# Performance work log

Hardware: AMD Instinct MI355X
Metric: run time of the kernel (lower is better)

The kernel has to match this reference:

```python
import jax, jax.numpy as jnp
import numpy as np
import math

# Instant-NGP hash grid config (matches init_kwargs)
L = 16            # num_levels
F = 2             # feature_dim
T = 524288        # table_size (2**19) per level
N_MIN = 16
N_MAX = 2048
N_PTS = 524288    # number of query points

# spatial-hash primes from Instant-NGP / tiny-cuda-nn
PRIMES = jnp.array([1, 2654435761, 805459861], dtype=jnp.uint32)


def setup_inputs() -> dict:
    key = jax.random.key(0)
    k1, k2 = jax.random.split(key)
    x = jax.random.uniform(k1, (N_PTS, 3), dtype=jnp.float32)  # coords in [0,1)^3
    # nn.initializers.uniform(scale=1e-4) -> U[0, 1e-4)
    hash_table = jax.random.uniform(k2, (L * T, F), dtype=jnp.float32) * 1e-4
    return {"x": x, "hash_table": hash_table}


def reference(x, hash_table):
    # per-level resolutions: floor(N_min * growth**level), growth per module setup()
    growth = math.exp((math.log(N_MAX) - math.log(N_MIN)) / (L - 1))
    scalings = jnp.floor(N_MIN * growth ** jnp.arange(L, dtype=jnp.float32))  # [L]

    scaled = x[:, None, :] * scalings[None, :, None]          # [N, L, 3]
    cell = jnp.floor(scaled)
    frac = scaled - cell                                      # [N, L, 3] trilinear fracs

    # 8 cube-corner binary offsets
    offs = jnp.array([[(i >> 2) & 1, (i >> 1) & 1, i & 1] for i in range(8)],
                     dtype=jnp.uint32)                        # [8, 3]

    corners = cell.astype(jnp.uint32)[:, :, None, :] + offs[None, None, :, :]  # [N, L, 8, 3]

    # spatial hash: (x*p0) ^ (y*p1) ^ (z*p2) mod T, wrapped uint32 arithmetic
    hp = corners * PRIMES                                     # [N, L, 8, 3] (wraps mod 2^32)
    h = hp[..., 0] ^ hp[..., 1] ^ hp[..., 2]                  # [N, L, 8]
    level_offset = (jnp.arange(L, dtype=jnp.uint32) * jnp.uint32(T))[None, :, None]
    idx = (h % jnp.uint32(T)) + level_offset                  # [N, L, 8] into full table

    feats = hash_table[idx]                                   # [N, L, 8, F] gather

    # trilinear weights: prod_d [ o*frac + (1-o)*(1-frac) ]
    offs_f = offs.astype(frac.dtype)[None, None]              # [1, 1, 8, 3]
    fr = frac[:, :, None, :]                                  # [N, L, 1, 3]
    w = jnp.prod(offs_f * fr + (1.0 - offs_f) * (1.0 - fr), axis=-1)  # [N, L, 8]

    out = jnp.sum(feats * w[..., None], axis=2)               # [N, L, F]
    return out.reshape(out.shape[0], L * F)                   # [N, L*F]
```

## Files before the change

kernel.cpp:

```cpp
#include <hip/hip_runtime.h>

__device__ __constant__ float c_scal[16] = {
    16.f, 22.f, 30.f, 42.f, 58.f, 80.f, 111.f, 153.f,
    212.f, 294.f, 406.f, 561.f, 776.f, 1072.f, 1482.f, 2047.f
};

#define TBL_T 524288u
#define NPTS  524288u
#define TMASK (TBL_T - 1u)

__device__ __forceinline__ float2 level_feat(
        const float2* __restrict__ tbl, float px, float py, float pz,
        float s, unsigned base) {
    float sx = px * s, sy = py * s, sz = pz * s;
    float cx = floorf(sx), cy = floorf(sy), cz = floorf(sz);
    float fx = sx - cx, fy = sy - cy, fz = sz - cz;

    unsigned ux = (unsigned)cx, uy = (unsigned)cy, uz = (unsigned)cz;

    unsigned hy0 = uy * 2654435761u, hy1 = (uy + 1u) * 2654435761u;
    unsigned hz0 = uz * 805459861u,  hz1 = (uz + 1u) * 805459861u;

    float wx1 = fx, wx0 = 1.f - fx;
    float wy1 = fy, wy0 = 1.f - fy;
    float wz1 = fz, wz0 = 1.f - fz;

    float wyz[4] = { wy0 * wz0, wy0 * wz1, wy1 * wz0, wy1 * wz1 };
    unsigned hyz[4] = { hy0 ^ hz0, hy0 ^ hz1, hy1 ^ hz0, hy1 ^ hz1 };

    float o0 = 0.f, o1 = 0.f;

    if ((ux & 1u) == 0u) {
        float4 f[4];
#pragma unroll
        for (int j = 0; j < 4; ++j) {
            unsigned idx0 = ((ux ^ hyz[j]) & TMASK) + base;
            f[j] = *reinterpret_cast<const float4*>(
                       reinterpret_cast<const float*>(tbl) + ((idx0 & ~1u) << 1));
        }
#pragma unroll
        for (int j = 0; j < 4; ++j) {
            unsigned idx0 = ((ux ^ hyz[j]) & TMASK) + base;
            bool hi0 = (idx0 & 1u) != 0u;
            float c0x = hi0 ? f[j].z : f[j].x;
            float c0y = hi0 ? f[j].w : f[j].y;
            float c1x = hi0 ? f[j].x : f[j].z;
            float c1y = hi0 ? f[j].y : f[j].w;
            o0 += c0x * (wx0 * wyz[j]) + c1x * (wx1 * wyz[j]);
            o1 += c0y * (wx0 * wyz[j]) + c1y * (wx1 * wyz[j]);
        }
    } else {
        unsigned ux1 = ux + 1u;
        float2 v0[4], v1[4];
#pragma unroll
        for (int j = 0; j < 4; ++j) {
            v0[j] = tbl[((ux  ^ hyz[j]) & TMASK) + base];
            v1[j] = tbl[((ux1 ^ hyz[j]) & TMASK) + base];
        }
#pragma unroll
        for (int j = 0; j < 4; ++j) {
            o0 += v0[j].x * (wx0 * wyz[j]) + v1[j].x * (wx1 * wyz[j]);
            o1 += v0[j].y * (wx0 * wyz[j]) + v1[j].y * (wx1 * wyz[j]);
        }
    }
    return make_float2(o0, o1);
}

__global__ __launch_bounds__(256) void hashenc_level(
        const float* __restrict__ x,
        const float2* __restrict__ tbl,
        float2* __restrict__ ws,
        int l) {
    unsigned p = blockIdx.x * 256u + threadIdx.x;
    float px = x[p * 3 + 0], py = x[p * 3 + 1], pz = x[p * 3 + 2];
    ws[(size_t)l * NPTS + p] =
        level_feat(tbl, px, py, pz, c_scal[l], (unsigned)l * TBL_T);
}

__global__ __launch_bounds__(256) void hashenc_coarse(
        const float* __restrict__ x,
        const float2* __restrict__ tbl,
        float2* __restrict__ ws) {
    unsigned p = blockIdx.x * 256u + threadIdx.x;
    float px = x[p * 3 + 0], py = x[p * 3 + 1], pz = x[p * 3 + 2];
#pragma unroll
    for (int l = 0; l < 5; ++l)
        ws[(size_t)l * NPTS + p] =
            level_feat(tbl, px, py, pz, c_scal[l], (unsigned)l * TBL_T);
}

__global__ __launch_bounds__(256) void hashenc_transpose(
        const float2* __restrict__ ws,
        float4* __restrict__ out) {
    unsigned p = blockIdx.x * 256u + threadIdx.x;
    float2 v[16];
#pragma unroll
    for (int l = 0; l < 16; ++l) v[l] = ws[(size_t)l * NPTS + p];
    float4* dst = out + (size_t)p * 8u;
#pragma unroll
    for (int q = 0; q < 8; ++q)
        dst[q] = make_float4(v[2 * q].x, v[2 * q].y, v[2 * q + 1].x, v[2 * q + 1].y);
}

__global__ __launch_bounds__(256) void hashenc_mono(
        const float* __restrict__ x,
        const float2* __restrict__ tbl,
        float4* __restrict__ out) {
    unsigned p = blockIdx.x * 256u + threadIdx.x;
    float px = x[p * 3 + 0], py = x[p * 3 + 1], pz = x[p * 3 + 2];
    float o[32];
#pragma unroll
    for (int l = 0; l < 16; ++l) {
        float2 f = level_feat(tbl, px, py, pz, c_scal[l], (unsigned)l * TBL_T);
        o[2 * l] = f.x; o[2 * l + 1] = f.y;
        __syncthreads();
    }
    float4* dst = out + (size_t)p * 8u;
#pragma unroll
    for (int q = 0; q < 8; ++q)
        dst[q] = make_float4(o[4 * q], o[4 * q + 1], o[4 * q + 2], o[4 * q + 3]);
}

extern "C" void kernel_launch(void* const* d_in, const int* in_sizes, int n_in,
                              void* d_out, int out_size, void* d_ws, size_t ws_size,
                              hipStream_t stream) {
    const float*  x   = (const float*)d_in[0];
    const float2* tbl = (const float2*)d_in[1];
    const size_t need = (size_t)16 * NPTS * sizeof(float2);

    const unsigned block = 256u;
    const unsigned grid  = NPTS / block;

    if (ws_size >= need) {
        float2* ws = (float2*)d_ws;
        hashenc_coarse<<<grid, block, 0, stream>>>(x, tbl, ws);
        for (int l = 5; l < 16; ++l)
            hashenc_level<<<grid, block, 0, stream>>>(x, tbl, ws, l);
        hashenc_transpose<<<grid, block, 0, stream>>>(ws, (float4*)d_out);
    } else {
        hashenc_mono<<<grid, block, 0, stream>>>(x, tbl, (float4*)d_out);
    }
}
```

Baseline: 244.3 us.

## Morton-sort query points and store per-level intermediates as packed bf16

```diff
diff --git a/kernel.cpp b/kernel.cpp
--- a/kernel.cpp
+++ b/kernel.cpp
@@ -8,6 +8,33 @@
 #define TBL_T 524288u
 #define NPTS  524288u
 #define TMASK (TBL_T - 1u)
+#define NBUCK 32768u
+
+__device__ __forceinline__ unsigned pack_bf2(float a, float b) {
+    unsigned ua = __float_as_uint(a), ub = __float_as_uint(b);
+    ua = (ua + 0x7FFFu + ((ua >> 16) & 1u)) >> 16;
+    ub = (ub + 0x7FFFu + ((ub >> 16) & 1u)) >> 16;
+    return ua | (ub << 16);
+}
+__device__ __forceinline__ float2 unpack_bf2(unsigned u) {
+    return make_float2(__uint_as_float(u << 16),
+                       __uint_as_float(u & 0xFFFF0000u));
+}
+
+__device__ __forceinline__ unsigned part1by2(unsigned v) {
+    v &= 0x3FFu;
+    v = (v | (v << 16)) & 0xFF0000FFu;
+    v = (v | (v << 8))  & 0x0F00F00Fu;
+    v = (v | (v << 4))  & 0xC30C30C3u;
+    v = (v | (v << 2))  & 0x49249249u;
+    return v;
+}
+__device__ __forceinline__ unsigned morton_key(float px, float py, float pz) {
+    unsigned kx = min(31u, (unsigned)(px * 32.f));
+    unsigned ky = min(31u, (unsigned)(py * 32.f));
+    unsigned kz = min(31u, (unsigned)(pz * 32.f));
+    return (part1by2(kx) << 2) | (part1by2(ky) << 1) | part1by2(kz);
+}
 
 __device__ __forceinline__ float2 level_feat(
         const float2* __restrict__ tbl, float px, float py, float pz,
@@ -66,48 +93,92 @@
     return make_float2(o0, o1);
 }
 
-__global__ __launch_bounds__(256) void hashenc_level(
-        const float* __restrict__ x,
-        const float2* __restrict__ tbl,
-        float2* __restrict__ ws,
-        int l) {
-    unsigned p = blockIdx.x * 256u + threadIdx.x;
-    float px = x[p * 3 + 0], py = x[p * 3 + 1], pz = x[p * 3 + 2];
-    ws[(size_t)l * NPTS + p] =
-        level_feat(tbl, px, py, pz, c_scal[l], (unsigned)l * TBL_T);
-}
-
-__global__ __launch_bounds__(256) void hashenc_coarse(
-        const float* __restrict__ x,
-        const float2* __restrict__ tbl,
-        float2* __restrict__ ws) {
-    unsigned p = blockIdx.x * 256u + threadIdx.x;
-    float px = x[p * 3 + 0], py = x[p * 3 + 1], pz = x[p * 3 + 2];
-#pragma unroll
-    for (int l = 0; l < 5; ++l)
-        ws[(size_t)l * NPTS + p] =
-            level_feat(tbl, px, py, pz, c_scal[l], (unsigned)l * TBL_T);
-}
-
-__global__ __launch_bounds__(256) void hashenc_transpose(
-        const float2* __restrict__ ws,
-        float4* __restrict__ out) {
-    unsigned p = blockIdx.x * 256u + threadIdx.x;
+__global__ __launch_bounds__(1024) void zero_hist(unsigned* __restrict__ h) {
+    h[blockIdx.x * 1024u + threadIdx.x] = 0u;
+}
+
+__global__ __launch_bounds__(256) void hist_k(
+        const float* __restrict__ x, unsigned* __restrict__ hist) {
+    unsigned p = blockIdx.x * 256u + threadIdx.x;
+    unsigned key = morton_key(x[p * 3], x[p * 3 + 1], x[p * 3 + 2]);
+    atomicAdd(&hist[key], 1u);
+}
+
+__global__ __launch_bounds__(1024) void scan32k(unsigned* __restrict__ hist) {
+    __shared__ unsigned part[1024];
+    unsigned t = threadIdx.x;
+    unsigned base = t * 32u;
+    unsigned vals[32]; unsigned sum = 0u;
+#pragma unroll
+    for (int i = 0; i < 32; ++i) { vals[i] = hist[base + i]; sum += vals[i]; }
+    part[t] = sum;
+    __syncthreads();
+    for (unsigned off = 1; off < 1024; off <<= 1) {
+        unsigned v = (t >= off) ? part[t - off] : 0u;
+        __syncthreads();
+        part[t] += v;
+        __syncthreads();
+    }
+    unsigned run = part[t] - sum;
+#pragma unroll
+    for (int i = 0; i < 32; ++i) { hist[base + i] = run; run += vals[i]; }
+}
+
+__global__ __launch_bounds__(256) void scatter_k(
+        const float* __restrict__ x, unsigned* __restrict__ cursor,
+        float4* __restrict__ xs4) {
+    unsigned p = blockIdx.x * 256u + threadIdx.x;
+    float px = x[p * 3], py = x[p * 3 + 1], pz = x[p * 3 + 2];
+    unsigned key = morton_key(px, py, pz);
+    unsigned pos = atomicAdd(&cursor[key], 1u);
+    xs4[pos] = make_float4(px, py, pz, __uint_as_float(p));
+}
+
+__global__ __launch_bounds__(256) void coarse_s(
+        const float4* __restrict__ xs4, const float2* __restrict__ tbl,
+        unsigned* __restrict__ slabs) {
+    unsigned p = blockIdx.x * 256u + threadIdx.x;
+    float4 X = xs4[p];
+#pragma unroll
+    for (int l = 0; l < 5; ++l) {
+        float2 f = level_feat(tbl, X.x, X.y, X.z, c_scal[l], (unsigned)l * TBL_T);
+        slabs[(size_t)l * NPTS + p] = pack_bf2(f.x, f.y);
+    }
+}
+
+__global__ __launch_bounds__(256) void level_s(
+        const float4* __restrict__ xs4, const float2* __restrict__ tbl,
+        unsigned* __restrict__ slabs, int l) {
+    unsigned p = blockIdx.x * 256u + threadIdx.x;
+    float4 X = xs4[p];
+    float2 f = level_feat(tbl, X.x, X.y, X.z, c_scal[l], (unsigned)l * TBL_T);
+    slabs[(size_t)l * NPTS + p] = pack_bf2(f.x, f.y);
+}
+
+__global__ __launch_bounds__(256) void last_s(
+        const float4* __restrict__ xs4, const float2* __restrict__ tbl,
+        const unsigned* __restrict__ slabs, float4* __restrict__ out) {
+    unsigned p = blockIdx.x * 256u + threadIdx.x;
+    float4 X = xs4[p];
+    float2 f15 = level_feat(tbl, X.x, X.y, X.z, c_scal[15], 15u * TBL_T);
+
     float2 v[16];
 #pragma unroll
-    for (int l = 0; l < 16; ++l) v[l] = ws[(size_t)l * NPTS + p];
-    float4* dst = out + (size_t)p * 8u;
+    for (int l = 0; l < 15; ++l) v[l] = unpack_bf2(slabs[(size_t)l * NPTS + p]);
+    v[15] = f15;
+
+    unsigned orig = __float_as_uint(X.w);
+    float4* dst = out + (size_t)orig * 8u;
 #pragma unroll
     for (int q = 0; q < 8; ++q)
         dst[q] = make_float4(v[2 * q].x, v[2 * q].y, v[2 * q + 1].x, v[2 * q + 1].y);
 }
 
 __global__ __launch_bounds__(256) void hashenc_mono(
-        const float* __restrict__ x,
-        const float2* __restrict__ tbl,
+        const float* __restrict__ x, const float2* __restrict__ tbl,
         float4* __restrict__ out) {
     unsigned p = blockIdx.x * 256u + threadIdx.x;
-    float px = x[p * 3 + 0], py = x[p * 3 + 1], pz = x[p * 3 + 2];
+    float px = x[p * 3], py = x[p * 3 + 1], pz = x[p * 3 + 2];
     float o[32];
 #pragma unroll
     for (int l = 0; l < 16; ++l) {
@@ -126,17 +197,28 @@
                               hipStream_t stream) {
     const float*  x   = (const float*)d_in[0];
     const float2* tbl = (const float2*)d_in[1];
-    const size_t need = (size_t)16 * NPTS * sizeof(float2);
+
+    const size_t off_xs4   = (size_t)NBUCK * 4u;
+    const size_t off_slabs = off_xs4 + (size_t)NPTS * 16u;
+    const size_t need      = off_slabs + (size_t)15 * NPTS * 4u;
 
     const unsigned block = 256u;
     const unsigned grid  = NPTS / block;
 
     if (ws_size >= need) {
-        float2* ws = (float2*)d_ws;
-        hashenc_coarse<<<grid, block, 0, stream>>>(x, tbl, ws);
-        for (int l = 5; l < 16; ++l)
-            hashenc_level<<<grid, block, 0, stream>>>(x, tbl, ws, l);
-        hashenc_transpose<<<grid, block, 0, stream>>>(ws, (float4*)d_out);
+        unsigned* hist = (unsigned*)d_ws;
+        float4*   xs4  = (float4*)((char*)d_ws + off_xs4);
+        unsigned* slabs= (unsigned*)((char*)d_ws + off_slabs);
+
+        zero_hist<<<NBUCK / 1024u, 1024, 0, stream>>>(hist);
+        hist_k   <<<grid, block, 0, stream>>>(x, hist);
+        scan32k  <<<1, 1024, 0, stream>>>(hist);
+        scatter_k<<<grid, block, 0, stream>>>(x, hist, xs4);
+
+        coarse_s <<<grid, block, 0, stream>>>(xs4, tbl, slabs);
+        for (int l = 5; l < 15; ++l)
+            level_s<<<grid, block, 0, stream>>>(xs4, tbl, slabs, l);
+        last_s   <<<grid, block, 0, stream>>>(xs4, tbl, slabs, (float4*)d_out);
     } else {
         hashenc_mono<<<grid, block, 0, stream>>>(x, tbl, (float4*)d_out);
     }
```

After: 272.1 us. 11.4% more time.
